# Kernel tuning notes

Measured on AMD Instinct MI355X. Metric: run time of the kernel, lower is better.

## Reference

```python
import jax, jax.numpy as jnp
import numpy as np

NUM_BASES = 64
DEGREE = 3
DOMAIN = (0.0, 1.0)


def bspline_basis(x, degree, knots):
    """Cox-de Boor B-spline basis.
    x: (...,) values in [0,1); knots: (num_bases+degree+1,)
    returns (..., num_bases) degree-`degree` basis values.
    """
    xe = x[..., None]
    # degree-0 indicator bases: (..., K-1)
    B = ((knots[:-1] <= xe) & (xe < knots[1:])).astype(x.dtype)
    for d in range(1, degree + 1):
        left = (xe - knots[:-(d + 1)]) / (knots[d:-1] - knots[:-(d + 1)]) * B[..., :-1]
        right = (knots[d + 1:] - xe) / (knots[d + 1:] - knots[1:-d]) * B[..., 1:]
        B = left + right
    return B  # (..., num_bases)


def setup_inputs() -> dict:
    key = jax.random.key(0)
    k0, k1, k2, k3 = jax.random.split(key, 4)
    batch, input_dim = 4096, 64
    widths = [256, 256, 64]
    x = jax.random.uniform(k0, (batch, input_dim), dtype=jnp.float32)
    # per-layer edge coefficients: (in_dim, out_dim, num_bases), ~randn like nn.Parameter(torch.randn(num_bases)) per edge
    C0 = jax.random.normal(k1, (input_dim, widths[0], NUM_BASES), dtype=jnp.float32)
    C1 = jax.random.normal(k2, (widths[0], widths[1], NUM_BASES), dtype=jnp.float32)
    C2 = jax.random.normal(k3, (widths[1], widths[2], NUM_BASES), dtype=jnp.float32)
    return {"x": x, "C0": C0, "C1": C1, "C2": C2}


def reference(x, C0, C1, C2):
    knots = jnp.linspace(DOMAIN[0], DOMAIN[1], NUM_BASES + DEGREE + 1, dtype=x.dtype)
    lo, hi = DOMAIN
    act = x
    for C in (C0, C1, C2):
        a = (act - lo) / (hi - lo)                 # domain normalization (identity for (0,1))
        basis = bspline_basis(a, DEGREE, knots)    # (B, in, num_bases)
        # edge output o[b,i,j] = <basis[b,i,:], C[i,j,:]>; pruning_mask is all-ones; then sum over i
        act = jnp.einsum('bik,ijk->bj', basis, C)  # (B, out)
    return jnp.squeeze(act)
```

## Files before the change

### kernel.cpp

```cpp
#include <hip/hip_runtime.h>


#define NBATCH 4096

typedef float f4a __attribute__((ext_vector_type(4), aligned(4)));

__device__ __forceinline__ float knotf(int m) {
    if (m == 67) return 1.0f;
    return (float)m * (1.0f / 67.0f);
}

__device__ __forceinline__ void basis4(float xf, int& t_out, float w[4]) {
#pragma clang fp contract(off)
    int t = (int)floorf(xf * 67.0f);
    t = t < 0 ? 0 : (t > 66 ? 66 : t);
    #pragma unroll
    for (int it = 0; it < 2; ++it) {
        if (t > 0 && xf < knotf(t)) --t;
        else if (t < 66 && xf >= knotf(t + 1)) ++t;
    }
    float W[7];
    #pragma unroll
    for (int j = 0; j < 7; ++j) W[j] = 0.0f;
    W[3] = 1.0f;
    #pragma unroll
    for (int d = 1; d <= 3; ++d) {
        #pragma unroll
        for (int j = 0; j <= 6 - d; ++j) {
            const int k = t - 3 + j;
            const float ka = knotf(k);
            const float kb = knotf(k + d);
            const float kc = knotf(k + d + 1);
            const float ke = knotf(k + 1);
            const float lt = ((xf - ka) / (kb - ka)) * W[j];
            const float rt = ((kc - xf) / (kc - ke)) * W[j + 1];
            W[j] = lt + rt;
        }
    }
    t_out = t;
    w[0] = W[0]; w[1] = W[1]; w[2] = W[2]; w[3] = W[3];
}

__device__ __forceinline__ void make_wk(float xf, float4& wv, int& kv) {
    float wp[4] = {0.f, 0.f, 0.f, 0.f};
    int k0 = 0;
    if (xf >= 0.0f && xf < 1.0f) {
        int t; float w[4];
        basis4(xf, t, w);
        k0 = t - 3;
        k0 = k0 < 0 ? 0 : (k0 > 60 ? 60 : k0);
        const int s = (t - 3) - k0;
        #pragma unroll
        for (int m = 0; m < 4; ++m) {
            const int r = m - s;
            wp[m] = (r >= 0 && r <= 3) ? w[r] : 0.0f;
        }
    }
    wv = make_float4(wp[0], wp[1], wp[2], wp[3]);
    kv = k0;
}

__global__ __launch_bounds__(256) void transpose_fast(
        const float* __restrict__ C0, const float* __restrict__ C1,
        const float* __restrict__ C2, float* __restrict__ Ct0,
        float* __restrict__ Ct1, float* __restrict__ Ct2) {
    __shared__ float t[64][65];
    const int bid = blockIdx.x, tid = threadIdx.x;
    const float* C; float* Ct; int OUT, i, jt;
    if (bid < 256)       { C = C0; Ct = Ct0; OUT = 256; i = bid >> 2;          jt = bid & 3; }
    else if (bid < 1280) { C = C1; Ct = Ct1; OUT = 256; i = (bid - 256) >> 2;  jt = (bid - 256) & 3; }
    else                 { C = C2; Ct = Ct2; OUT = 64;  i = bid - 1280;        jt = 0; }
    const int j0 = jt * 64;
    const float* src = C + ((size_t)i * OUT + j0) * 64;
    float* dst = Ct + (size_t)i * 64 * OUT + j0;

    const int kq  = tid & 15;
    const int jl0 = tid >> 4;
    #pragma unroll
    for (int p = 0; p < 4; ++p) {
        const int jl = jl0 + 16 * p;
        const f4a v = *(const f4a*)(src + (size_t)jl * 64 + kq * 4);
        t[kq * 4 + 0][jl] = v[0];
        t[kq * 4 + 1][jl] = v[1];
        t[kq * 4 + 2][jl] = v[2];
        t[kq * 4 + 3][jl] = v[3];
    }
    __syncthreads();
    const int jq  = tid & 15;
    const int kl0 = tid >> 4;
    #pragma unroll
    for (int p = 0; p < 4; ++p) {
        const int k = kl0 + 16 * p;
        f4a o;
        o[0] = t[k][jq * 4 + 0];
        o[1] = t[k][jq * 4 + 1];
        o[2] = t[k][jq * 4 + 2];
        o[3] = t[k][jq * 4 + 3];
        *(f4a*)(dst + (size_t)k * OUT + jq * 4) = o;
    }
}

__device__ __forceinline__ int compact_wave(int lane, int passes,
        float4* __restrict__ wbuf, int* __restrict__ kbuf, int mult) {
    int base = 0;
    for (int p = 0; p < passes; ++p) {
        const int e = 64 * p + lane;
        const float4 wv = wbuf[e];
        const int    kv = kbuf[e];
        const bool act = (wv.x != 0.f) || (wv.y != 0.f) ||
                         (wv.z != 0.f) || (wv.w != 0.f);
        const unsigned long long mask = __ballot(act);
        const int pos = base + (int)__popcll(mask & ((1ull << lane) - 1ull));
        if (act) { wbuf[pos] = wv; kbuf[pos] = (e * 64 + kv) * mult; }
        base += (int)__popcll(mask);
    }
    return base;
}

__device__ __forceinline__ void gather_list(const float* __restrict__ Ct,
        const float4* __restrict__ wl, const int* __restrict__ rl,
        int cnt, int j0, double acc[4]) {
    if (cnt <= 0) return;
    f4a c0[4], c1[4];
    {
        const int r0 = __builtin_amdgcn_readfirstlane(rl[0]);
        const float* p = Ct + r0 + j0;
        c0[0] = *(const f4a*)(p);       c0[1] = *(const f4a*)(p + 256);
        c0[2] = *(const f4a*)(p + 512); c0[3] = *(const f4a*)(p + 768);
    }
    {
        const int e1 = (cnt > 1) ? 1 : 0;
        const int r1 = __builtin_amdgcn_readfirstlane(rl[e1]);
        const float* p = Ct + r1 + j0;
        c1[0] = *(const f4a*)(p);       c1[1] = *(const f4a*)(p + 256);
        c1[2] = *(const f4a*)(p + 512); c1[3] = *(const f4a*)(p + 768);
    }
    for (int e = 0; e < cnt; ++e) {
        const int ep = (e + 2 < cnt) ? e + 2 : cnt - 1;
        const int rN = __builtin_amdgcn_readfirstlane(rl[ep]);
        f4a c2[4];
        {
            const float* p = Ct + rN + j0;
            c2[0] = *(const f4a*)(p);       c2[1] = *(const f4a*)(p + 256);
            c2[2] = *(const f4a*)(p + 512); c2[3] = *(const f4a*)(p + 768);
        }
        const float4 wv = wl[e];
        const double w0 = (double)wv.x, w1 = (double)wv.y;
        const double w2 = (double)wv.z, w3 = (double)wv.w;
        #pragma unroll
        for (int ee = 0; ee < 4; ++ee) {
            acc[ee] = fma(w0, (double)c0[0][ee], acc[ee]);
            acc[ee] = fma(w1, (double)c0[1][ee], acc[ee]);
            acc[ee] = fma(w2, (double)c0[2][ee], acc[ee]);
            acc[ee] = fma(w3, (double)c0[3][ee], acc[ee]);
        }
        #pragma unroll
        for (int r = 0; r < 4; ++r) { c0[r] = c1[r]; c1[r] = c2[r]; }
    }
}

__global__ __launch_bounds__(256) void kan_mega3(
        const float* __restrict__ x,
        const float* __restrict__ Ct0,
        const float* __restrict__ Ct1,
        const float* __restrict__ Ct2,
        float* __restrict__ out) {
    __shared__ __align__(16) float4 wtab[4][256];
    __shared__ int                  ktab[4][256];
    __shared__ int scnt[4];

    const int tid  = threadIdx.x;
    const int lane = tid & 63;
    const int wx   = tid >> 6;
    const int b    = blockIdx.x * 4 + wx;
    const int j0   = lane * 4;

    {
        float4 wv; int kv;
        make_wk(x[(size_t)b * 64 + lane], wv, kv);
        wtab[wx][lane] = wv;
        ktab[wx][lane] = (lane * 64 + kv) * 256;
    }
    double acc1[4] = {0.0, 0.0, 0.0, 0.0};
    gather_list(Ct0, &wtab[wx][0], &ktab[wx][0], 64, j0, acc1);

    #pragma unroll
    for (int e = 0; e < 4; ++e) {
        float4 wv; int kv;
        make_wk((float)acc1[e], wv, kv);
        wtab[wx][j0 + e] = wv;
        ktab[wx][j0 + e] = kv;
    }
    const int cnt2 = compact_wave(lane, 4, &wtab[wx][0], &ktab[wx][0], 256);

    double acc2[4] = {0.0, 0.0, 0.0, 0.0};
    gather_list(Ct1, &wtab[wx][0], &ktab[wx][0], cnt2, j0, acc2);

    #pragma unroll
    for (int e = 0; e < 4; ++e) {
        float4 wv; int kv;
        make_wk((float)acc2[e], wv, kv);
        wtab[wx][j0 + e] = wv;
        ktab[wx][j0 + e] = kv;
    }
    const int cnt3 = compact_wave(lane, 4, &wtab[wx][0], &ktab[wx][0], 64);
    if (lane == 0) scnt[wx] = cnt3;
    __syncthreads();
    if (wx != 0) return;

    const int bsub = lane >> 4;
    const int jq   = lane & 15;
    const int cn   = scnt[bsub];
    const int cmax = max(max(scnt[0], scnt[1]), max(scnt[2], scnt[3]));
    double a3[4] = {0.0, 0.0, 0.0, 0.0};

    if (cmax > 0) {
        auto ldb = [&](int e, f4a p[4], float4& wv) {
            const int ec = (cn > 0) ? ((e < cn) ? e : cn - 1) : 0;
            wv = (cn > 0) ? wtab[bsub][ec] : make_float4(0.f, 0.f, 0.f, 0.f);
            int ro = (cn > 0) ? ktab[bsub][ec] : 0;
            if (e >= cn) wv = make_float4(0.f, 0.f, 0.f, 0.f);
            const float* pb = Ct2 + ro + jq * 4;
            p[0] = *(const f4a*)(pb);
            p[1] = *(const f4a*)(pb + 64);
            p[2] = *(const f4a*)(pb + 128);
            p[3] = *(const f4a*)(pb + 192);
        };
        f4a P0[4], P1[4]; float4 W0, W1;
        ldb(0, P0, W0);
        ldb(1, P1, W1);
        for (int e = 0; e < cmax; ++e) {
            f4a P2[4]; float4 W2;
            ldb(e + 2, P2, W2);
            const double w0 = (double)W0.x, w1 = (double)W0.y;
            const double w2 = (double)W0.z, w3 = (double)W0.w;
            #pragma unroll
            for (int ee = 0; ee < 4; ++ee) {
                a3[ee] = fma(w0, (double)P0[0][ee], a3[ee]);
                a3[ee] = fma(w1, (double)P0[1][ee], a3[ee]);
                a3[ee] = fma(w2, (double)P0[2][ee], a3[ee]);
                a3[ee] = fma(w3, (double)P0[3][ee], a3[ee]);
            }
            #pragma unroll
            for (int r = 0; r < 4; ++r) { P0[r] = P1[r]; P1[r] = P2[r]; }
            W0 = W1; W1 = W2;
        }
    }

    const float4 o = make_float4((float)a3[0], (float)a3[1],
                                 (float)a3[2], (float)a3[3]);
    *(float4*)(out + (size_t)(blockIdx.x * 4 + bsub) * 64 + jq * 4) = o;
}


__device__ __forceinline__ void stage1(float xf, float sw[4], int& st) {
    const bool inr = (xf >= 0.0f) && (xf < 1.0f);
    if (!inr) { st = -1; sw[0] = sw[1] = sw[2] = sw[3] = 0.0f; return; }
    int t; float w[4];
    basis4(xf, t, w);
    sw[0] = w[0]; sw[1] = w[1]; sw[2] = w[2]; sw[3] = w[3];
    st = t;
}

template<int IN, int OUT>
__device__ __forceinline__ float gather_acc(const float* __restrict__ C, int j,
                                            const float (*__restrict__ sw)[4],
                                            const int* __restrict__ st) {
    double acc = 0.0;
    for (int i = 0; i < IN; ++i) {
        const int t = st[i];
        if (t < 0) continue;
        const float* Crow = C + ((size_t)i * OUT + j) * 64;
        #pragma unroll
        for (int r = 0; r < 4; ++r) {
            const int k4 = t - 3 + r;
            if (k4 >= 0 && k4 <= 63)
                acc += (double)sw[i][r] * (double)Crow[k4];
        }
    }
    return (float)acc;
}

__global__ __launch_bounds__(256) void kan_fused(const float* __restrict__ x,
                                                 const float* __restrict__ C0,
                                                 const float* __restrict__ C1,
                                                 const float* __restrict__ C2,
                                                 float* __restrict__ out) {
    __shared__ float cur[256];
    __shared__ float sw[256][4];
    __shared__ int   st[256];
    const int b = blockIdx.x, tid = threadIdx.x;

    if (tid < 64) stage1(x[(size_t)b * 64 + tid], sw[tid], st[tid]);
    __syncthreads();
    {
        const float a = gather_acc<64, 256>(C0, tid, sw, st);
        __syncthreads();
        cur[tid] = a;
    }
    __syncthreads();

    stage1(cur[tid], sw[tid], st[tid]);
    __syncthreads();
    {
        const float a = gather_acc<256, 256>(C1, tid, sw, st);
        __syncthreads();
        cur[tid] = a;
    }
    __syncthreads();

    stage1(cur[tid], sw[tid], st[tid]);
    __syncthreads();
    if (tid < 64) out[(size_t)b * 64 + tid] = gather_acc<256, 64>(C2, tid, sw, st);
}


extern "C" void kernel_launch(void* const* d_in, const int* in_sizes, int n_in,
                              void* d_out, int out_size, void* d_ws, size_t ws_size,
                              hipStream_t stream) {
    const float* x  = (const float*)d_in[0];
    const float* C0 = (const float*)d_in[1];
    const float* C1 = (const float*)d_in[2];
    const float* C2 = (const float*)d_in[3];
    float* out = (float*)d_out;

    const size_t CT1 = (size_t)256 * 64 * 256 * 4;
    const size_t CT0 = (size_t)64  * 64 * 256 * 4;
    const size_t CT2 = (size_t)256 * 64 * 64  * 4;
    const size_t need = CT1 + CT0 + CT2;

    if (ws_size >= need) {
        float* ct1 = (float*)d_ws;
        float* ct0 = (float*)((char*)d_ws + CT1);
        float* ct2 = (float*)((char*)d_ws + CT1 + CT0);

        transpose_fast<<<1536, 256, 0, stream>>>(C0, C1, C2, ct0, ct1, ct2);
        kan_mega3<<<1024, 256, 0, stream>>>(x, ct0, ct1, ct2, out);
    } else {
        kan_fused<<<NBATCH, 256, 0, stream>>>(x, C0, C1, C2, out);
    }
}
```

Measured before the change: 185.4 us.

## Fuse coefficient transpose and KAN layers into one cooperative kernel with grid sync

Merges the transpose kernel and the three-layer KAN kernel into a single cooperative launch. Blocks first transpose coefficient tiles in a grid-stride loop, then pass a grid-wide barrier, then run the layer gathers. Shared memory is reused between the two phases. The aim is to remove one kernel launch and the gap between kernels, at the cost of a grid barrier and a requirement that all 1024 blocks be co-resident; if the cooperative launch fails it falls back to the old two-kernel path.

```diff
diff --git a/kernel.cpp b/kernel.cpp
--- a/kernel.cpp
+++ b/kernel.cpp
@@ -1,4 +1,7 @@
 #include <hip/hip_runtime.h>
+#include <hip/hip_cooperative_groups.h>
+
+namespace cg = cooperative_groups;
 
 
 #define NBATCH 4096
@@ -60,6 +63,207 @@
     kv = k0;
 }
 
+__device__ __forceinline__ int compact_wave(int lane, int passes,
+        float4* __restrict__ wbuf, int* __restrict__ kbuf, int mult) {
+    int base = 0;
+    for (int p = 0; p < passes; ++p) {
+        const int e = 64 * p + lane;
+        const float4 wv = wbuf[e];
+        const int    kv = kbuf[e];
+        const bool act = (wv.x != 0.f) || (wv.y != 0.f) ||
+                         (wv.z != 0.f) || (wv.w != 0.f);
+        const unsigned long long mask = __ballot(act);
+        const int pos = base + (int)__popcll(mask & ((1ull << lane) - 1ull));
+        if (act) { wbuf[pos] = wv; kbuf[pos] = (e * 64 + kv) * mult; }
+        base += (int)__popcll(mask);
+    }
+    return base;
+}
+
+__device__ __forceinline__ void gather_list(const float* __restrict__ Ct,
+        const float4* __restrict__ wl, const int* __restrict__ rl,
+        int cnt, int j0, double acc[4]) {
+    if (cnt <= 0) return;
+    f4a c0[4], c1[4];
+    {
+        const int r0 = __builtin_amdgcn_readfirstlane(rl[0]);
+        const float* p = Ct + r0 + j0;
+        c0[0] = *(const f4a*)(p);       c0[1] = *(const f4a*)(p + 256);
+        c0[2] = *(const f4a*)(p + 512); c0[3] = *(const f4a*)(p + 768);
+    }
+    {
+        const int e1 = (cnt > 1) ? 1 : 0;
+        const int r1 = __builtin_amdgcn_readfirstlane(rl[e1]);
+        const float* p = Ct + r1 + j0;
+        c1[0] = *(const f4a*)(p);       c1[1] = *(const f4a*)(p + 256);
+        c1[2] = *(const f4a*)(p + 512); c1[3] = *(const f4a*)(p + 768);
+    }
+    for (int e = 0; e < cnt; ++e) {
+        const int ep = (e + 2 < cnt) ? e + 2 : cnt - 1;
+        const int rN = __builtin_amdgcn_readfirstlane(rl[ep]);
+        f4a c2[4];
+        {
+            const float* p = Ct + rN + j0;
+            c2[0] = *(const f4a*)(p);       c2[1] = *(const f4a*)(p + 256);
+            c2[2] = *(const f4a*)(p + 512); c2[3] = *(const f4a*)(p + 768);
+        }
+        const float4 wv = wl[e];
+        const double w0 = (double)wv.x, w1 = (double)wv.y;
+        const double w2 = (double)wv.z, w3 = (double)wv.w;
+        #pragma unroll
+        for (int ee = 0; ee < 4; ++ee) {
+            acc[ee] = fma(w0, (double)c0[0][ee], acc[ee]);
+            acc[ee] = fma(w1, (double)c0[1][ee], acc[ee]);
+            acc[ee] = fma(w2, (double)c0[2][ee], acc[ee]);
+            acc[ee] = fma(w3, (double)c0[3][ee], acc[ee]);
+        }
+        #pragma unroll
+        for (int r = 0; r < 4; ++r) { c0[r] = c1[r]; c1[r] = c2[r]; }
+    }
+}
+
+__global__ __launch_bounds__(256) void kan_all(
+        const float* __restrict__ x,
+        const float* __restrict__ C0, const float* __restrict__ C1,
+        const float* __restrict__ C2,
+        float* __restrict__ Ct0,
+        float* __restrict__ Ct1,
+        float* __restrict__ Ct2,
+        float* __restrict__ out) {
+    __shared__ __align__(16) char shmem[20512];
+
+    const int bid = blockIdx.x, tid = threadIdx.x;
+
+    {
+        float (*t)[65] = reinterpret_cast<float (*)[65]>(shmem);
+        for (int u = bid; u < 1536; u += 1024) {
+            const float* C; float* Ct; int OUT, i, jt;
+            if (u < 256)       { C = C0; Ct = Ct0; OUT = 256; i = u >> 2;         jt = u & 3; }
+            else if (u < 1280) { C = C1; Ct = Ct1; OUT = 256; i = (u - 256) >> 2; jt = (u - 256) & 3; }
+            else               { C = C2; Ct = Ct2; OUT = 64;  i = u - 1280;       jt = 0; }
+            const int j0t = jt * 64;
+            const float* src = C + ((size_t)i * OUT + j0t) * 64;
+            float* dst = Ct + (size_t)i * 64 * OUT + j0t;
+
+            const int kq  = tid & 15;
+            const int jl0 = tid >> 4;
+            #pragma unroll
+            for (int p = 0; p < 4; ++p) {
+                const int jl = jl0 + 16 * p;
+                const f4a v = *(const f4a*)(src + (size_t)jl * 64 + kq * 4);
+                t[kq * 4 + 0][jl] = v[0];
+                t[kq * 4 + 1][jl] = v[1];
+                t[kq * 4 + 2][jl] = v[2];
+                t[kq * 4 + 3][jl] = v[3];
+            }
+            __syncthreads();
+            const int jq  = tid & 15;
+            const int kl0 = tid >> 4;
+            #pragma unroll
+            for (int p = 0; p < 4; ++p) {
+                const int k = kl0 + 16 * p;
+                f4a o;
+                o[0] = t[k][jq * 4 + 0];
+                o[1] = t[k][jq * 4 + 1];
+                o[2] = t[k][jq * 4 + 2];
+                o[3] = t[k][jq * 4 + 3];
+                *(f4a*)(dst + (size_t)k * OUT + jq * 4) = o;
+            }
+            __syncthreads();
+        }
+    }
+    __threadfence();
+    cg::this_grid().sync();
+
+    float4* wtab = reinterpret_cast<float4*>(shmem);
+    int*    ktab = reinterpret_cast<int*>(shmem + 16384);
+    int*    scnt = reinterpret_cast<int*>(shmem + 16384 + 4096);
+
+    const int lane = tid & 63;
+    const int wx   = tid >> 6;
+    const int b    = bid * 4 + wx;
+    const int j0   = lane * 4;
+    float4* wt = wtab + wx * 256;
+    int*    kt = ktab + wx * 256;
+
+    {
+        float4 wv; int kv;
+        make_wk(x[(size_t)b * 64 + lane], wv, kv);
+        wt[lane] = wv;
+        kt[lane] = (lane * 64 + kv) * 256;
+    }
+    double acc1[4] = {0.0, 0.0, 0.0, 0.0};
+    gather_list(Ct0, wt, kt, 64, j0, acc1);
+
+    #pragma unroll
+    for (int e = 0; e < 4; ++e) {
+        float4 wv; int kv;
+        make_wk((float)acc1[e], wv, kv);
+        wt[j0 + e] = wv;
+        kt[j0 + e] = kv;
+    }
+    const int cnt2 = compact_wave(lane, 4, wt, kt, 256);
+
+    double acc2[4] = {0.0, 0.0, 0.0, 0.0};
+    gather_list(Ct1, wt, kt, cnt2, j0, acc2);
+
+    #pragma unroll
+    for (int e = 0; e < 4; ++e) {
+        float4 wv; int kv;
+        make_wk((float)acc2[e], wv, kv);
+        wt[j0 + e] = wv;
+        kt[j0 + e] = kv;
+    }
+    const int cnt3 = compact_wave(lane, 4, wt, kt, 64);
+    if (lane == 0) scnt[wx] = cnt3;
+    __syncthreads();
+    if (wx != 0) return;
+
+    const int bsub = lane >> 4;
+    const int jq   = lane & 15;
+    const int cn   = scnt[bsub];
+    const int cmax = max(max(scnt[0], scnt[1]), max(scnt[2], scnt[3]));
+    double a3[4] = {0.0, 0.0, 0.0, 0.0};
+
+    if (cmax > 0) {
+        auto ldb = [&](int e, f4a p[4], float4& wv) {
+            const int ec = (cn > 0) ? ((e < cn) ? e : cn - 1) : 0;
+            wv = (cn > 0) ? wtab[bsub * 256 + ec] : make_float4(0.f, 0.f, 0.f, 0.f);
+            int ro = (cn > 0) ? ktab[bsub * 256 + ec] : 0;
+            if (e >= cn) wv = make_float4(0.f, 0.f, 0.f, 0.f);
+            const float* pb = Ct2 + ro + jq * 4;
+            p[0] = *(const f4a*)(pb);
+            p[1] = *(const f4a*)(pb + 64);
+            p[2] = *(const f4a*)(pb + 128);
+            p[3] = *(const f4a*)(pb + 192);
+        };
+        f4a P0[4], P1[4]; float4 W0, W1;
+        ldb(0, P0, W0);
+        ldb(1, P1, W1);
+        for (int e = 0; e < cmax; ++e) {
+            f4a P2[4]; float4 W2;
+            ldb(e + 2, P2, W2);
+            const double w0 = (double)W0.x, w1 = (double)W0.y;
+            const double w2 = (double)W0.z, w3 = (double)W0.w;
+            #pragma unroll
+            for (int ee = 0; ee < 4; ++ee) {
+                a3[ee] = fma(w0, (double)P0[0][ee], a3[ee]);
+                a3[ee] = fma(w1, (double)P0[1][ee], a3[ee]);
+                a3[ee] = fma(w2, (double)P0[2][ee], a3[ee]);
+                a3[ee] = fma(w3, (double)P0[3][ee], a3[ee]);
+            }
+            #pragma unroll
+            for (int r = 0; r < 4; ++r) { P0[r] = P1[r]; P1[r] = P2[r]; }
+            W0 = W1; W1 = W2;
+        }
+    }
+
+    const float4 o = make_float4((float)a3[0], (float)a3[1],
+                                 (float)a3[2], (float)a3[3]);
+    *(float4*)(out + (size_t)(bid * 4 + bsub) * 64 + jq * 4) = o;
+}
+
+
 __global__ __launch_bounds__(256) void transpose_fast(
         const float* __restrict__ C0, const float* __restrict__ C1,
         const float* __restrict__ C2, float* __restrict__ Ct0,
@@ -100,70 +304,9 @@
     }
 }
 
-__device__ __forceinline__ int compact_wave(int lane, int passes,
-        float4* __restrict__ wbuf, int* __restrict__ kbuf, int mult) {
-    int base = 0;
-    for (int p = 0; p < passes; ++p) {
-        const int e = 64 * p + lane;
-        const float4 wv = wbuf[e];
-        const int    kv = kbuf[e];
-        const bool act = (wv.x != 0.f) || (wv.y != 0.f) ||
-                         (wv.z != 0.f) || (wv.w != 0.f);
-        const unsigned long long mask = __ballot(act);
-        const int pos = base + (int)__popcll(mask & ((1ull << lane) - 1ull));
-        if (act) { wbuf[pos] = wv; kbuf[pos] = (e * 64 + kv) * mult; }
-        base += (int)__popcll(mask);
-    }
-    return base;
-}
-
-__device__ __forceinline__ void gather_list(const float* __restrict__ Ct,
-        const float4* __restrict__ wl, const int* __restrict__ rl,
-        int cnt, int j0, double acc[4]) {
-    if (cnt <= 0) return;
-    f4a c0[4], c1[4];
-    {
-        const int r0 = __builtin_amdgcn_readfirstlane(rl[0]);
-        const float* p = Ct + r0 + j0;
-        c0[0] = *(const f4a*)(p);       c0[1] = *(const f4a*)(p + 256);
-        c0[2] = *(const f4a*)(p + 512); c0[3] = *(const f4a*)(p + 768);
-    }
-    {
-        const int e1 = (cnt > 1) ? 1 : 0;
-        const int r1 = __builtin_amdgcn_readfirstlane(rl[e1]);
-        const float* p = Ct + r1 + j0;
-        c1[0] = *(const f4a*)(p);       c1[1] = *(const f4a*)(p + 256);
-        c1[2] = *(const f4a*)(p + 512); c1[3] = *(const f4a*)(p + 768);
-    }
-    for (int e = 0; e < cnt; ++e) {
-        const int ep = (e + 2 < cnt) ? e + 2 : cnt - 1;
-        const int rN = __builtin_amdgcn_readfirstlane(rl[ep]);
-        f4a c2[4];
-        {
-            const float* p = Ct + rN + j0;
-            c2[0] = *(const f4a*)(p);       c2[1] = *(const f4a*)(p + 256);
-            c2[2] = *(const f4a*)(p + 512); c2[3] = *(const f4a*)(p + 768);
-        }
-        const float4 wv = wl[e];
-        const double w0 = (double)wv.x, w1 = (double)wv.y;
-        const double w2 = (double)wv.z, w3 = (double)wv.w;
-        #pragma unroll
-        for (int ee = 0; ee < 4; ++ee) {
-            acc[ee] = fma(w0, (double)c0[0][ee], acc[ee]);
-            acc[ee] = fma(w1, (double)c0[1][ee], acc[ee]);
-            acc[ee] = fma(w2, (double)c0[2][ee], acc[ee]);
-            acc[ee] = fma(w3, (double)c0[3][ee], acc[ee]);
-        }
-        #pragma unroll
-        for (int r = 0; r < 4; ++r) { c0[r] = c1[r]; c1[r] = c2[r]; }
-    }
-}
-
 __global__ __launch_bounds__(256) void kan_mega3(
-        const float* __restrict__ x,
-        const float* __restrict__ Ct0,
-        const float* __restrict__ Ct1,
-        const float* __restrict__ Ct2,
+        const float* __restrict__ x, const float* __restrict__ Ct0,
+        const float* __restrict__ Ct1, const float* __restrict__ Ct2,
         float* __restrict__ out) {
     __shared__ __align__(16) float4 wtab[4][256];
     __shared__ int                  ktab[4][256];
@@ -334,8 +477,14 @@
         float* ct0 = (float*)((char*)d_ws + CT1);
         float* ct2 = (float*)((char*)d_ws + CT1 + CT0);
 
-        transpose_fast<<<1536, 256, 0, stream>>>(C0, C1, C2, ct0, ct1, ct2);
-        kan_mega3<<<1024, 256, 0, stream>>>(x, ct0, ct1, ct2, out);
+        void* args[] = {(void*)&x, (void*)&C0, (void*)&C1, (void*)&C2,
+                        (void*)&ct0, (void*)&ct1, (void*)&ct2, (void*)&out};
+        hipError_t err = hipLaunchCooperativeKernel(
+            (const void*)kan_all, dim3(1024), dim3(256), args, 0, stream);
+        if (err != hipSuccess) {
+            transpose_fast<<<1536, 256, 0, stream>>>(C0, C1, C2, ct0, ct1, ct2);
+            kan_mega3<<<1024, 256, 0, stream>>>(x, ct0, ct1, ct2, out);
+        }
     } else {
         kan_fused<<<NBATCH, 256, 0, stream>>>(x, C0, C1, C2, out);
     }
```

Result: slower. 402.7 us (+117.2%).
